# Optimization experiments

Hardware: AMD Instinct MI355X
Metric: run time of the kernel (lower is better)

## Reference

```python
import jax, jax.numpy as jnp
import numpy as np

N, E, CN, CE = 2048, 8192, 256, 256
MN, ME = 16384, 65536
RATIO = 0.5
K_KEEP = int(np.ceil(RATIO * N))  # 1024, static


def _glorot(key, shape):
    lim = float(np.sqrt(6.0 / (shape[0] + shape[1])))
    return jax.random.uniform(key, shape, jnp.float32, -lim, lim)


def setup_inputs() -> dict:
    key = jax.random.key(0)
    ks = jax.random.split(key, 16)
    return {
        "x_n": jax.random.normal(ks[0], (N, CN), jnp.float32),
        "edge_index_n": jax.random.randint(ks[1], (2, MN), 0, N),
        "edge_weight_n": jax.random.uniform(ks[2], (MN,), jnp.float32),
        "x_e": jax.random.normal(ks[3], (E, CE), jnp.float32),
        "edge_index_e": jax.random.randint(ks[4], (2, ME), 0, E),
        "edge_weight_e": jax.random.uniform(ks[5], (ME,), jnp.float32),
        "edge_index": jax.random.randint(ks[6], (2, E), 0, N),
        "n_batch": jnp.zeros((N,), jnp.int64 if jax.config.jax_enable_x64 else jnp.int32),
        "e_batch": jnp.zeros((E,), jnp.int64 if jax.config.jax_enable_x64 else jnp.int32),
        "x_n0": jax.random.normal(ks[7], (N, CN), jnp.float32),
        "x_e0": jax.random.normal(ks[8], (E, CE), jnp.float32),
        # HodgeLaguerreConv(in, 1, K=2) params for node- and edge-scoring GNNs
        "W_n0": _glorot(ks[9], (CN, 1)),
        "W_n1": _glorot(ks[10], (CN, 1)),
        "b_n": jnp.zeros((1,), jnp.float32),
        "W_e0": _glorot(ks[11], (CE, 1)),
        "W_e1": _glorot(ks[12], (CE, 1)),
        "b_e": jnp.zeros((1,), jnp.float32),
    }


def _hodge_conv_k2(x, ei, ew, W0, W1, b):
    # PyG: out = lin0(T0) + lin1(T1), T0 = x, T1 = x - L@x (propagate: dst += w_e * x[src])
    n = x.shape[0]
    agg = jax.ops.segment_sum(ew[:, None] * x[ei[0]], ei[1], num_segments=n)
    return x @ W0 + (x - agg) @ W1 + b


def reference(x_n, edge_index_n, edge_weight_n, x_e, edge_index_e, edge_weight_e,
              edge_index, n_batch, e_batch, x_n0, x_e0,
              W_n0, W_n1, b_n, W_e0, W_e1, b_e):
    score_n = jax.nn.sigmoid(_hodge_conv_k2(x_n, edge_index_n, edge_weight_n, W_n0, W_n1, b_n).reshape(-1))
    score_e = jax.nn.sigmoid(_hodge_conv_k2(x_e, edge_index_e, edge_weight_e, W_e0, W_e1, b_e).reshape(-1))
    xns = x_n * score_n[:, None]
    xes = x_e * score_e[:, None]
    # incidence matrix B (par1): B[src,e]=-1, B[dst,e]=+1 (duplicates summed, as torch sparse)
    src, dst = edge_index[0], edge_index[1]
    eidx = jnp.arange(E)
    par1 = jnp.zeros((N, E), x_n.dtype).at[src, eidx].add(-1.0).at[dst, eidx].add(1.0)
    par1_abs = jnp.zeros((N, E), x_n.dtype).at[src, eidx].add(1.0).at[dst, eidx].add(1.0)
    # joint node score with 0.125 * |B| @ score_e
    joint = score_n + 0.125 * (par1_abs @ score_e)
    perm = jnp.argsort(-joint)                # descending
    idx_keep = jnp.sort(perm[:K_KEEP])        # kept nodes in original order (boolean-mask order)
    mask_n = jnp.zeros((N,), x_n.dtype).at[idx_keep].set(1.0)
    # edges touching any removed node get nonzero; keep edges where this is exactly 0
    removed_hits = par1_abs.T @ (1.0 - mask_n)
    keep_e = (removed_hits == 0.0).astype(x_n.dtype)     # [E]
    # masked incidence: kept-node rows, removed-edge columns zeroed
    par_masked = par1[idx_keep] * keep_e[None, :]        # [k, E]
    L0 = par_masked @ par_masked.T                       # [k, k]  (equals compacted L0)
    L1 = par_masked.T @ par_masked                       # [E, E]  (zero rows/cols at removed edges)
    # eigsh(L0, k=1, 'LM'): max eigenvalue; scipy path is non-differentiable -> stop_gradient
    lam = jax.lax.stop_gradient(jnp.linalg.eigvalsh(L0)[-1])
    L0s = 2.0 * L0 / lam
    L1s = 2.0 * L1 / lam
    x_n_out = xns[idx_keep]
    x_e_out = xes * keep_e[:, None]
    x_n0_out = x_n0[idx_keep]
    x_e0_out = x_e0 * keep_e[:, None]
    return (x_n_out, L0s, x_e_out, L1s, par_masked, x_n0_out, x_e0_out)
```

## Files before the change

kernel.cpp:

```cpp
#include <hip/hip_runtime.h>
#include <math.h>

#define NN   2048
#define EE   8192
#define CNF  256
#define MN   16384
#define ME   65536
#define KK   1024

#define OUT_XN   ((size_t)0)
#define OUT_L0   ((size_t)262144)
#define OUT_XE   ((size_t)1310720)
#define OUT_L1   ((size_t)3407872)
#define OUT_PM   ((size_t)70516736)
#define OUT_XN0  ((size_t)78905344)
#define OUT_XE0  ((size_t)79167488)

#define WS_T1N    0
#define WS_SLINN  2048
#define WS_T1E    4096
#define WS_SLINE  12288
#define WS_SCN    20480
#define WS_SCE    22528
#define WS_JOINT  30720
#define WS_AGGN   32768
#define WS_AGGE   34816
#define WS_LAM    43008
#define WS_IDXK   43520
#define WS_RANK   44544
#define WS_OFFS   47616
#define WS_ADJE   66176
#define WS_KEEPE  82560

#define DCAP  8
#define PWR_T 64
#define RBAD  0xFFFFu

typedef float vf4 __attribute__((ext_vector_type(4)));

__global__ void k_prep(const float* __restrict__ xn, const float* __restrict__ xe,
                       const float* __restrict__ Wn0, const float* __restrict__ Wn1,
                       const float* __restrict__ We0, const float* __restrict__ We1,
                       float* __restrict__ wsf) {
    if (blockIdx.x == 0) {
        for (int i = threadIdx.x; i < 2048; i += 256) wsf[WS_AGGN + i] = 0.f;
        for (int i = threadIdx.x; i < 8192; i += 256) wsf[WS_AGGE + i] = 0.f;
        for (int i = threadIdx.x; i < 2048; i += 256) wsf[WS_JOINT + i] = 0.f;
    }
    int gw = (blockIdx.x * blockDim.x + threadIdx.x) >> 6;
    int lane = threadIdx.x & 63;
    int wstr = (gridDim.x * blockDim.x) >> 6;
    for (int row = gw; row < NN + EE; row += wstr) {
        const float *x, *W0, *W1; float *t1, *sl; int r;
        if (row < NN) { r = row;      x = xn + (size_t)r * CNF; W0 = Wn0; W1 = Wn1; t1 = wsf + WS_T1N; sl = wsf + WS_SLINN; }
        else          { r = row - NN; x = xe + (size_t)r * CNF; W0 = We0; W1 = We1; t1 = wsf + WS_T1E; sl = wsf + WS_SLINE; }
        float4 xv = ((const float4*)x)[lane];
        float4 w0 = ((const float4*)W0)[lane];
        float4 w1 = ((const float4*)W1)[lane];
        float d0 = xv.x*w0.x + xv.y*w0.y + xv.z*w0.z + xv.w*w0.w;
        float d1 = xv.x*w1.x + xv.y*w1.y + xv.z*w1.z + xv.w*w1.w;
        #pragma unroll
        for (int o = 32; o > 0; o >>= 1) { d0 += __shfl_down(d0, o, 64); d1 += __shfl_down(d1, o, 64); }
        if (lane == 0) { t1[r] = d1; sl[r] = d0 + d1; }
    }
}

__global__ void k_agg(const int* __restrict__ ein, const float* __restrict__ ewn,
                      const int* __restrict__ eie, const float* __restrict__ ewe,
                      float* __restrict__ wsf) {
    int i = blockIdx.x * blockDim.x + threadIdx.x;
    if (i < MN) {
        int s = ein[i], d = ein[MN + i];
        atomicAdd(wsf + WS_AGGN + d, ewn[i] * wsf[WS_T1N + s]);
    }
    if (i < ME) {
        int s = eie[i], d = eie[ME + i];
        atomicAdd(wsf + WS_AGGE + d, ewe[i] * wsf[WS_T1E + s]);
    }
}

__global__ void k_score(const int* __restrict__ ei,
                        const float* __restrict__ bn, const float* __restrict__ be,
                        float* __restrict__ wsf) {
    int i = blockIdx.x * blockDim.x + threadIdx.x;
    if (i < NN) {
        float z = wsf[WS_SLINN + i] - wsf[WS_AGGN + i] + bn[0];
        float s = 1.0f / (1.0f + expf(-z));
        wsf[WS_SCN + i] = s;
        atomicAdd(wsf + WS_JOINT + i, s);
    }
    if (i < EE) {
        float z = wsf[WS_SLINE + i] - wsf[WS_AGGE + i] + be[0];
        float s = 1.0f / (1.0f + expf(-z));
        wsf[WS_SCE + i] = s;
        float v = 0.125f * s;
        atomicAdd(wsf + WS_JOINT + ei[i], v);
        atomicAdd(wsf + WS_JOINT + ei[EE + i], v);
    }
}

__device__ __forceinline__ float block_reduce_sum_1b(float val, float* red) {
    #pragma unroll
    for (int o = 32; o > 0; o >>= 1) val += __shfl_down(val, o, 64);
    int lane = threadIdx.x & 63, wid = threadIdx.x >> 6;
    if (lane == 0) red[wid] = val;
    __syncthreads();
    float r = 0.0f;
    #pragma unroll
    for (int j = 0; j < 16; ++j) r += red[j];
    return r;
}

__device__ __forceinline__ int block_incl_scan_1024(int v, int* t16) {
    int lane = threadIdx.x & 63, wid = threadIdx.x >> 6;
    int x = v;
    #pragma unroll
    for (int o = 1; o < 64; o <<= 1) {
        int t = __shfl_up(x, o, 64);
        if (lane >= o) x += t;
    }
    if (lane == 63) t16[wid] = x;
    __syncthreads();
    if (threadIdx.x < 16) {
        int w = t16[threadIdx.x];
        #pragma unroll
        for (int o = 1; o < 16; o <<= 1) {
            int t = __shfl_up(w, o, 16);
            if ((int)threadIdx.x >= o) w += t;
        }
        t16[threadIdx.x] = w;
    }
    __syncthreads();
    int base = wid ? t16[wid - 1] : 0;
    return base + x;
}

__global__ __launch_bounds__(1024) void k_mid(
        const int* __restrict__ ei,
        float* __restrict__ out, float* __restrict__ wsf, int* __restrict__ wsi) {
    int tid = threadIdx.x;
    if (blockIdx.x != 0) {
        size_t w = (size_t)(blockIdx.x - 1) * 1024 + tid;
        size_t ws = (size_t)(gridDim.x - 1) * 1024;
        vf4 z = (vf4)(0.0f);
        vf4* l1 = (vf4*)(out + OUT_L1);
        for (size_t p = w; p < (size_t)EE * EE / 4; p += ws) __builtin_nontemporal_store(z, &l1[p]);
        vf4* pm = (vf4*)(out + OUT_PM);
        for (size_t p = w; p < (size_t)KK * EE / 4; p += ws) __builtin_nontemporal_store(z, &pm[p]);
        vf4* l0 = (vf4*)(out + OUT_L0);
        for (size_t p = w; p < (size_t)KK * KK / 4; p += ws) __builtin_nontemporal_store(z, &l0[p]);
        vf4* xe_ = (vf4*)(out + OUT_XE);
        for (size_t p = w; p < (size_t)EE * CNF / 4; p += ws) __builtin_nontemporal_store(z, &xe_[p]);
        vf4* xe0_ = (vf4*)(out + OUT_XE0);
        for (size_t p = w; p < (size_t)EE * CNF / 4; p += ws) __builtin_nontemporal_store(z, &xe0_[p]);
        return;
    }
    __shared__ unsigned long long s_u64[2048];
    __shared__ unsigned short s_rank[2048];
    __shared__ unsigned short s_adjo[16384 + DCAP];
    __shared__ float s_red[16];
    __shared__ int s_t16[16];
    int* s_i = (int*)s_u64;

    unsigned long long k0, k1;
    {
        int i0 = 2 * tid, i1 = 2 * tid + 1;
        float f0 = wsf[WS_JOINT + i0], f1 = wsf[WS_JOINT + i1];
        unsigned u0 = __float_as_uint(f0), u1 = __float_as_uint(f1);
        unsigned sk0 = (u0 & 0x80000000u) ? ~u0 : (u0 | 0x80000000u);
        unsigned sk1 = (u1 & 0x80000000u) ? ~u1 : (u1 | 0x80000000u);
        k0 = (((unsigned long long)sk0) << 11) | (unsigned long long)(2047 - i0);
        k1 = (((unsigned long long)sk1) << 11) | (unsigned long long)(2047 - i1);
    }
    unsigned long long prefix = 0ULL;
    int rem = KK;
    #pragma unroll
    for (int p = 5; p >= 0; --p) {
        __syncthreads();
        if (tid < 256) s_i[tid] = 0;
        __syncthreads();
        int sh = p << 3;
        unsigned long long ph = prefix >> (sh + 8);
        if ((k0 >> (sh + 8)) == ph) atomicAdd(&s_i[(int)((k0 >> sh) & 255)], 1);
        if ((k1 >> (sh + 8)) == ph) atomicAdd(&s_i[(int)((k1 >> sh) & 255)], 1);
        __syncthreads();
        if (tid < 64) {
            int b0 = s_i[4 * tid + 0], b1 = s_i[4 * tid + 1];
            int b2 = s_i[4 * tid + 2], b3 = s_i[4 * tid + 3];
            int sl = b0 + b1 + b2 + b3;
            int si = sl;
            #pragma unroll
            for (int o = 1; o < 64; o <<= 1) {
                int t = __shfl_down(si, o, 64);
                if (tid + o < 64) si += t;
            }
            int sup = si - sl;
            int sg3 = sup;
            int sg2 = sg3 + b3;
            int sg1 = sg2 + b2;
            int sg0 = sg1 + b1;
            if (sg0 < rem && rem <= sg0 + b0) { s_i[256] = (tid << 2) | 0; s_i[257] = rem - sg0; }
            if (sg1 < rem && rem <= sg1 + b1) { s_i[256] = (tid << 2) | 1; s_i[257] = rem - sg1; }
            if (sg2 < rem && rem <= sg2 + b2) { s_i[256] = (tid << 2) | 2; s_i[257] = rem - sg2; }
            if (sg3 < rem && rem <= sg3 + b3) { s_i[256] = (tid << 2) | 3; s_i[257] = rem - sg3; }
        }
        __syncthreads();
        prefix |= ((unsigned long long)(unsigned)s_i[256]) << sh;
        rem = s_i[257];
    }
    {
        int a0 = (k0 >= prefix) ? 1 : 0;
        int a1 = (k1 >= prefix) ? 1 : 0;
        int pr = a0 + a1;
        __syncthreads();
        int incl = block_incl_scan_1024(pr, s_t16);
        int excl = incl - pr;
        int i0 = 2 * tid, i1 = 2 * tid + 1;
        int r0 = excl, r1 = excl + a0;
        s_rank[i0] = a0 ? (unsigned short)r0 : (unsigned short)RBAD;
        s_rank[i1] = a1 ? (unsigned short)r1 : (unsigned short)RBAD;
        wsi[WS_RANK + i0] = a0 ? r0 : -1;
        wsi[WS_RANK + i1] = a1 ? r1 : -1;
        if (a0) wsi[WS_IDXK + r0] = i0;
        if (a1) wsi[WS_IDXK + r1] = i1;
    }
    __syncthreads();

    s_i[tid] = 0;
    __syncthreads();
    for (int e = tid; e < EE; e += 1024) {
        int s = ei[e], d = ei[EE + e];
        unsigned rs = s_rank[s], rd = s_rank[d];
        int kept = (rs != RBAD && rd != RBAD);
        wsi[WS_KEEPE + e] = kept;
        if (kept && s != d) {
            atomicAdd(&s_i[(int)rs], 1);
            atomicAdd(&s_i[(int)rd], 1);
        }
    }
    __syncthreads();

    {
        int dg = s_i[tid];
        int incl = block_incl_scan_1024(dg, s_t16);
        int offs = incl - dg;
        s_i[2048 + tid] = offs;
        wsi[WS_OFFS + tid] = offs;
        if (tid == 1023) wsi[WS_OFFS + 1024] = incl;
    }
    __syncthreads();

    for (int e = tid; e < EE; e += 1024) {
        int s = ei[e], d = ei[EE + e];
        unsigned rs = s_rank[s], rd = s_rank[d];
        if (rs != RBAD && rd != RBAD && s != d) {
            int p = atomicAdd(&s_i[2048 + (int)rs], 1);
            s_adjo[p] = (unsigned short)rd;
            wsi[WS_ADJE + p] = (e << 1);
            int q = atomicAdd(&s_i[2048 + (int)rd], 1);
            s_adjo[q] = (unsigned short)rs;
            wsi[WS_ADJE + q] = (e << 1) | 1;
        }
    }
    __syncthreads();

    {
        int o0 = wsi[WS_OFFS + tid];
        int d  = wsi[WS_OFFS + tid + 1] - o0;
        __syncthreads();
        float* v0 = (float*)s_u64;
        float* v1 = v0 + 1024;
        unsigned h = (unsigned)tid * 2654435761u + 911u;
        h ^= h >> 15; h *= 2246822519u; h ^= h >> 13;
        v0[tid] = (float)(h & 0xFFFFu) * (1.0f / 65536.0f) - 0.5f;
        int aj[DCAP];
        #pragma unroll
        for (int j = 0; j < DCAP; ++j) aj[j] = (j < d) ? (int)s_adjo[o0 + j] : 0;
        __syncthreads();
        float* vc = v0; float* vn = v1;
        for (int iter = 0; iter < PWR_T; ++iter) {
            float acc = 0.0f;
            #pragma unroll
            for (int j = 0; j < DCAP; ++j) acc += (j < d) ? vc[aj[j]] : 0.0f;
            for (int i = o0 + DCAP; i < o0 + d; ++i) acc += vc[(int)s_adjo[i]];
            float y = (float)d * vc[tid] - acc;
            if ((iter & 7) == 7) {
                float n2 = block_reduce_sum_1b(y * y, s_red);
                y *= (n2 > 0.0f) ? rsqrtf(n2) : 0.0f;
            }
            vn[tid] = y;
            __syncthreads();
            float* tmp = vc; vc = vn; vn = tmp;
        }
        float acc = 0.0f;
        #pragma unroll
        for (int j = 0; j < DCAP; ++j) acc += (j < d) ? vc[aj[j]] : 0.0f;
        for (int i = o0 + DCAP; i < o0 + d; ++i) acc += vc[(int)s_adjo[i]];
        float y = (float)d * vc[tid] - acc;
        float rq = block_reduce_sum_1b(vc[tid] * y, s_red);
        if (tid == 0) wsf[WS_LAM] = rq;
    }
}

__global__ __launch_bounds__(1024) void k_final(
        const float* __restrict__ xn, const float* __restrict__ xe,
        const float* __restrict__ xn0, const float* __restrict__ xe0,
        const int* __restrict__ ei,
        float* __restrict__ out, const float* __restrict__ wsf,
        const int* __restrict__ wsi) {
    float sc = 2.0f / wsf[WS_LAM];
    int gt = blockIdx.x * 1024 + threadIdx.x;
    int gstr = gridDim.x * 1024;

    for (int i = gt; i < KK * 64; i += gstr) {
        int r = i >> 6, c = i & 63;
        int src = wsi[WS_IDXK + r];
        float s = wsf[WS_SCN + src];
        float4 v = ((const float4*)(xn + (size_t)src * CNF))[c];
        v.x *= s; v.y *= s; v.z *= s; v.w *= s;
        ((float4*)(out + OUT_XN))[(size_t)r * 64 + c] = v;
        ((float4*)(out + OUT_XN0))[(size_t)r * 64 + c] = ((const float4*)(xn0 + (size_t)src * CNF))[c];
    }
    for (int i = gt; i < EE * 64; i += gstr) {
        int e = i >> 6;
        if (!wsi[WS_KEEPE + e]) continue;
        int c = i & 63;
        float s = wsf[WS_SCE + e];
        float4 v = ((const float4*)(xe + (size_t)e * CNF))[c];
        v.x *= s; v.y *= s; v.z *= s; v.w *= s;
        ((float4*)(out + OUT_XE))[(size_t)e * 64 + c] = v;
        ((float4*)(out + OUT_XE0))[(size_t)e * 64 + c] = ((const float4*)(xe0 + (size_t)e * CNF))[c];
    }
    {
        float* pm = out + OUT_PM;
        float* L0 = out + OUT_L0;
        for (int e = gt; e < EE; e += gstr) {
            int s = ei[e], d = ei[EE + e];
            int rs = wsi[WS_RANK + s], rd = wsi[WS_RANK + d];
            if (rs < 0 || rd < 0 || s == d) continue;
            pm[(size_t)rs * EE + e] = -1.0f;
            pm[(size_t)rd * EE + e] =  1.0f;
            atomicAdd(&L0[(size_t)rs * KK + rs],  sc);
            atomicAdd(&L0[(size_t)rd * KK + rd],  sc);
            atomicAdd(&L0[(size_t)rs * KK + rd], -sc);
            atomicAdd(&L0[(size_t)rd * KK + rs], -sc);
        }
    }
    {
        float* L1 = out + OUT_L1;
        int gwv = gt >> 6, lane = gt & 63, wstr = gstr >> 6;
        for (int r = gwv; r < KK; r += wstr) {
            int o0 = wsi[WS_OFFS + r], o1 = wsi[WS_OFFS + r + 1];
            for (int i = o0; i < o1; ++i) {
                int eiv = wsi[WS_ADJE + i];
                int e = eiv >> 1;
                float si = (eiv & 1) ? sc : -sc;
                for (int j = o0 + lane; j < o1; j += 64) {
                    int ejv = wsi[WS_ADJE + j];
                    atomicAdd(&L1[(size_t)e * EE + (ejv >> 1)], (ejv & 1) ? si : -si);
                }
            }
        }
    }
}

extern "C" void kernel_launch(void* const* d_in, const int* in_sizes, int n_in,
                              void* d_out, int out_size, void* d_ws, size_t ws_size,
                              hipStream_t stream) {
    const float* x_n  = (const float*)d_in[0];
    const int*   ei_n = (const int*)  d_in[1];
    const float* ew_n = (const float*)d_in[2];
    const float* x_e  = (const float*)d_in[3];
    const int*   ei_e = (const int*)  d_in[4];
    const float* ew_e = (const float*)d_in[5];
    const int*   ei   = (const int*)  d_in[6];
    const float* x_n0 = (const float*)d_in[9];
    const float* x_e0 = (const float*)d_in[10];
    const float* Wn0  = (const float*)d_in[11];
    const float* Wn1  = (const float*)d_in[12];
    const float* bn   = (const float*)d_in[13];
    const float* We0  = (const float*)d_in[14];
    const float* We1  = (const float*)d_in[15];
    const float* be   = (const float*)d_in[16];

    float* out = (float*)d_out;
    float* wsf = (float*)d_ws;
    int*   wsi = (int*)d_ws;

    k_prep <<<640, 256, 0, stream>>>(x_n, x_e, Wn0, Wn1, We0, We1, wsf);
    k_agg  <<<256, 256, 0, stream>>>(ei_n, ew_n, ei_e, ew_e, wsf);
    k_score<<<32, 256, 0, stream>>>(ei, bn, be, wsf);
    k_mid  <<<256, 1024, 0, stream>>>(ei, out, wsf, wsi);
    k_final<<<256, 1024, 0, stream>>>(x_n, x_e, x_n0, x_e0, ei, out, wsf, wsi);
}
```

Baseline: 432.1 us.

## Move power iteration out of k_mid to overlap with feature gather/pm writes

The eigenvalue power iteration moves from the tail of the single-block k_mid into block 0 of a new k_final1 kernel. The other blocks of that kernel do the feature gathers and incidence writes at the same time, so the serial power iteration no longer leaves the GPU idle. The L0/L1 atomics that need lambda go into a separate k_final2 launch. Neighbour ranks are packed into the upper bits of the adjacency workspace entries, which requires masking the edge id when decoding, and the change adds one extra kernel launch.

```diff
diff --git a/kernel.cpp b/kernel.cpp
--- a/kernel.cpp
+++ b/kernel.cpp
@@ -157,8 +157,6 @@
     }
     __shared__ unsigned long long s_u64[2048];
     __shared__ unsigned short s_rank[2048];
-    __shared__ unsigned short s_adjo[16384 + DCAP];
-    __shared__ float s_red[16];
     __shared__ int s_t16[16];
     int* s_i = (int*)s_u64;
 
@@ -255,29 +253,38 @@
         unsigned rs = s_rank[s], rd = s_rank[d];
         if (rs != RBAD && rd != RBAD && s != d) {
             int p = atomicAdd(&s_i[2048 + (int)rs], 1);
-            s_adjo[p] = (unsigned short)rd;
-            wsi[WS_ADJE + p] = (e << 1);
+            wsi[WS_ADJE + p] = ((int)rd << 14) | (e << 1);
             int q = atomicAdd(&s_i[2048 + (int)rd], 1);
-            s_adjo[q] = (unsigned short)rs;
-            wsi[WS_ADJE + q] = (e << 1) | 1;
-        }
-    }
-    __syncthreads();
-
-    {
+            wsi[WS_ADJE + q] = ((int)rs << 14) | (e << 1) | 1;
+        }
+    }
+}
+
+__global__ __launch_bounds__(1024) void k_final1(
+        const float* __restrict__ xn, const float* __restrict__ xe,
+        const float* __restrict__ xn0, const float* __restrict__ xe0,
+        const int* __restrict__ ei,
+        float* __restrict__ out, float* __restrict__ wsf,
+        const int* __restrict__ wsi) {
+    __shared__ unsigned short s_adjo[16384];
+    __shared__ float s_v0[1024], s_v1[1024];
+    __shared__ float s_red[16];
+    int tid = threadIdx.x;
+
+    if (blockIdx.x == 0) {
+        int total = wsi[WS_OFFS + 1024];
+        for (int i = tid; i < total; i += 1024)
+            s_adjo[i] = (unsigned short)(((unsigned)wsi[WS_ADJE + i]) >> 14);
         int o0 = wsi[WS_OFFS + tid];
         int d  = wsi[WS_OFFS + tid + 1] - o0;
-        __syncthreads();
-        float* v0 = (float*)s_u64;
-        float* v1 = v0 + 1024;
         unsigned h = (unsigned)tid * 2654435761u + 911u;
         h ^= h >> 15; h *= 2246822519u; h ^= h >> 13;
-        v0[tid] = (float)(h & 0xFFFFu) * (1.0f / 65536.0f) - 0.5f;
+        s_v0[tid] = (float)(h & 0xFFFFu) * (1.0f / 65536.0f) - 0.5f;
+        __syncthreads();
         int aj[DCAP];
         #pragma unroll
         for (int j = 0; j < DCAP; ++j) aj[j] = (j < d) ? (int)s_adjo[o0 + j] : 0;
-        __syncthreads();
-        float* vc = v0; float* vn = v1;
+        float* vc = s_v0; float* vn = s_v1;
         for (int iter = 0; iter < PWR_T; ++iter) {
             float acc = 0.0f;
             #pragma unroll
@@ -299,18 +306,11 @@
         float y = (float)d * vc[tid] - acc;
         float rq = block_reduce_sum_1b(vc[tid] * y, s_red);
         if (tid == 0) wsf[WS_LAM] = rq;
-    }
-}
-
-__global__ __launch_bounds__(1024) void k_final(
-        const float* __restrict__ xn, const float* __restrict__ xe,
-        const float* __restrict__ xn0, const float* __restrict__ xe0,
-        const int* __restrict__ ei,
-        float* __restrict__ out, const float* __restrict__ wsf,
-        const int* __restrict__ wsi) {
-    float sc = 2.0f / wsf[WS_LAM];
-    int gt = blockIdx.x * 1024 + threadIdx.x;
-    int gstr = gridDim.x * 1024;
+        return;
+    }
+
+    int gt = (blockIdx.x - 1) * 1024 + tid;
+    int gstr = (gridDim.x - 1) * 1024;
 
     for (int i = gt; i < KK * 64; i += gstr) {
         int r = i >> 6, c = i & 63;
@@ -333,13 +333,30 @@
     }
     {
         float* pm = out + OUT_PM;
-        float* L0 = out + OUT_L0;
         for (int e = gt; e < EE; e += gstr) {
             int s = ei[e], d = ei[EE + e];
             int rs = wsi[WS_RANK + s], rd = wsi[WS_RANK + d];
             if (rs < 0 || rd < 0 || s == d) continue;
             pm[(size_t)rs * EE + e] = -1.0f;
             pm[(size_t)rd * EE + e] =  1.0f;
+        }
+    }
+}
+
+__global__ __launch_bounds__(1024) void k_final2(
+        const int* __restrict__ ei,
+        float* __restrict__ out, const float* __restrict__ wsf,
+        const int* __restrict__ wsi) {
+    float sc = 2.0f / wsf[WS_LAM];
+    int gt = blockIdx.x * 1024 + threadIdx.x;
+    int gstr = gridDim.x * 1024;
+
+    {
+        float* L0 = out + OUT_L0;
+        for (int e = gt; e < EE; e += gstr) {
+            int s = ei[e], d = ei[EE + e];
+            int rs = wsi[WS_RANK + s], rd = wsi[WS_RANK + d];
+            if (rs < 0 || rd < 0 || s == d) continue;
             atomicAdd(&L0[(size_t)rs * KK + rs],  sc);
             atomicAdd(&L0[(size_t)rd * KK + rd],  sc);
             atomicAdd(&L0[(size_t)rs * KK + rd], -sc);
@@ -353,11 +370,11 @@
             int o0 = wsi[WS_OFFS + r], o1 = wsi[WS_OFFS + r + 1];
             for (int i = o0; i < o1; ++i) {
                 int eiv = wsi[WS_ADJE + i];
-                int e = eiv >> 1;
+                int e = (eiv >> 1) & 0x1FFF;
                 float si = (eiv & 1) ? sc : -sc;
                 for (int j = o0 + lane; j < o1; j += 64) {
                     int ejv = wsi[WS_ADJE + j];
-                    atomicAdd(&L1[(size_t)e * EE + (ejv >> 1)], (ejv & 1) ? si : -si);
+                    atomicAdd(&L1[(size_t)e * EE + ((ejv >> 1) & 0x1FFF)], (ejv & 1) ? si : -si);
                 }
             }
         }
@@ -387,9 +404,10 @@
     float* wsf = (float*)d_ws;
     int*   wsi = (int*)d_ws;
 
-    k_prep <<<640, 256, 0, stream>>>(x_n, x_e, Wn0, Wn1, We0, We1, wsf);
-    k_agg  <<<256, 256, 0, stream>>>(ei_n, ew_n, ei_e, ew_e, wsf);
-    k_score<<<32, 256, 0, stream>>>(ei, bn, be, wsf);
-    k_mid  <<<256, 1024, 0, stream>>>(ei, out, wsf, wsi);
-    k_final<<<256, 1024, 0, stream>>>(x_n, x_e, x_n0, x_e0, ei, out, wsf, wsi);
-}
+    k_prep  <<<640, 256, 0, stream>>>(x_n, x_e, Wn0, Wn1, We0, We1, wsf);
+    k_agg   <<<256, 256, 0, stream>>>(ei_n, ew_n, ei_e, ew_e, wsf);
+    k_score <<<32, 256, 0, stream>>>(ei, bn, be, wsf);
+    k_mid   <<<256, 1024, 0, stream>>>(ei, out, wsf, wsi);
+    k_final1<<<256, 1024, 0, stream>>>(x_n, x_e, x_n0, x_e0, ei, out, wsf, wsi);
+    k_final2<<<256, 1024, 0, stream>>>(ei, out, wsf, wsi);
+}
```

Result: slower. 461.6 us (+6.8%).
